# Performance work log

Measured on AMD Instinct MI355X. Metric: run time of the kernel, lower is better.

## Reference

```python
import jax, jax.numpy as jnp
import numpy as np

EMBED_DIM = 768
NUM_HEADS = 12


def setup_inputs() -> dict:
    key = jax.random.key(0)
    k_x, k_w1, k_b1, k_w2, k_b2 = jax.random.split(key, 5)
    B, S, D = 4, 2048, EMBED_DIM
    s1 = 1.0 / np.sqrt(D)
    return {
        "x": jax.random.normal(k_x, (B, S, D), dtype=jnp.float32),
        "W1": jax.random.uniform(k_w1, (D, 3 * D), jnp.float32, -s1, s1),  # proj1 weight (in,out)
        "b1": jax.random.uniform(k_b1, (3 * D,), jnp.float32, -s1, s1),
        "W2": jax.random.uniform(k_w2, (D, D), jnp.float32, -s1, s1),  # proj2 weight (in,out)
        "b2": jax.random.uniform(k_b2, (D,), jnp.float32, -s1, s1),
    }


def reference(x, W1, b1, W2, b2):
    B, S, D = x.shape
    H = NUM_HEADS
    h = D // H
    qkv = x @ W1 + b1                       # [B,S,3D]
    qkv = qkv.reshape(B, S, H, 3 * h).transpose(0, 2, 1, 3)  # [B,H,S,3h]
    # chunk order in the original: K, Q, V
    K = qkv[..., :h]
    Q = qkv[..., h:2 * h]
    V = qkv[..., 2 * h:]
    # NOTE: original code computes Q @ V^T (not Q @ K^T) -- reproduced faithfully
    scores = jnp.einsum("bhqd,bhkd->bhqk", Q, V) / jnp.sqrt(jnp.float32(h))
    att = jax.nn.softmax(scores, axis=-1)
    out = jnp.einsum("bhqk,bhkd->bhqd", att, V)  # [B,H,S,h]
    out = out.transpose(0, 2, 1, 3).reshape(B, S, D)
    return out @ W2 + b2
```

## Files before the change

kernel.cpp:

```cpp
#include <hip/hip_runtime.h>
#include <hip/hip_bf16.h>
#include <math.h>


#define SEQ   2048
#define DIM   768
#define NHEAD 12
#define HDIM  64
#define BATCH 4

#define QSCALE 0.1803368801111244f

typedef __attribute__((ext_vector_type(8))) short s16x8;
typedef __attribute__((ext_vector_type(4))) float f32x4;

#if __has_builtin(__builtin_amdgcn_exp2f)
#define EXP2F(x) __builtin_amdgcn_exp2f(x)
#else
#define EXP2F(x) exp2f(x)
#endif

__device__ __forceinline__ unsigned short f2bf(float f) {
    union { float f; unsigned int u; } v; v.f = f;
    unsigned int r = v.u + 0x7fffu + ((v.u >> 16) & 1u);
    return (unsigned short)(r >> 16);
}

__device__ __forceinline__ void gload_lds16(const void* g, void* l) {
    __builtin_amdgcn_global_load_lds(
        (const __attribute__((address_space(1))) unsigned int*)g,
        (__attribute__((address_space(3))) unsigned int*)l, 16, 0, 0);
}

__global__ __launch_bounds__(256) void cvt_x(const float* __restrict__ x,
                                             unsigned short* __restrict__ xb)
{
    const size_t i4 = ((size_t)blockIdx.x * 256 + threadIdx.x) * 4;
    float4 v = *(const float4*)&x[i4];
    ushort4 o;
    o.x = f2bf(v.x); o.y = f2bf(v.y); o.z = f2bf(v.z); o.w = f2bf(v.w);
    *(ushort4*)&xb[i4] = o;
}

__global__ __launch_bounds__(256) void cvt_wt(const float* __restrict__ W,
                                              unsigned short* __restrict__ out,
                                              int src_ld, int qvmap)
{
    __shared__ float T[32][33];
    const int n0 = blockIdx.x * 32, k0 = blockIdx.y * 32;
    const int c0 = qvmap ? ((n0 >> 7) * 192 + 64 + (n0 & 127)) : n0;
    const int tc = threadIdx.x & 31, tr = threadIdx.x >> 5;
    #pragma unroll
    for (int i = 0; i < 4; ++i)
        T[tr + i * 8][tc] = W[(size_t)(k0 + tr + i * 8) * src_ld + c0 + tc];
    __syncthreads();
    #pragma unroll
    for (int i = 0; i < 4; ++i)
        out[(size_t)(n0 + tr + i * 8) * DIM + k0 + tc] = f2bf(T[tc][tr + i * 8]);
}

__device__ __forceinline__ void gemm128_loop(
    const unsigned short* __restrict__ A, const unsigned short* __restrict__ B,
    unsigned short* As, unsigned short* Bs, int m0, int n0, f32x4 acc[4][4])
{
    const int tid  = threadIdx.x;
    const int wave = tid >> 6;
    const int lane = tid & 63;
    const int quad = lane >> 4;
    const int lcol = lane & 15;
    const int wm = wave >> 1, wn = wave & 1;

    const int sr = lane >> 2;
    const int sp = lane & 3;
    const int sc = sp ^ ((sr >> 1) & 3);

    const int aswz = ((quad ^ ((lcol >> 1) & 3)) << 4);

    for (int k0 = 0; k0 < DIM; k0 += 32) {
        #pragma unroll
        for (int s = 0; s < 2; ++s) {
            const int r0 = wave * 32 + s * 16;
            gload_lds16(&A[(size_t)(m0 + r0 + sr) * DIM + k0 + sc * 8],
                        (void*)&As[r0 * 32]);
            gload_lds16(&B[(size_t)(n0 + r0 + sr) * DIM + k0 + sc * 8],
                        (void*)&Bs[r0 * 32]);
        }
        __syncthreads();

        s16x8 af[4], bf[4];
        #pragma unroll
        for (int mt = 0; mt < 4; ++mt) {
            const int row = wm * 64 + mt * 16 + lcol;
            af[mt] = *(const s16x8*)((const char*)As + row * 64 + aswz);
        }
        #pragma unroll
        for (int nt = 0; nt < 4; ++nt) {
            const int row = wn * 64 + nt * 16 + lcol;
            bf[nt] = *(const s16x8*)((const char*)Bs + row * 64 + aswz);
        }
        #pragma unroll
        for (int mt = 0; mt < 4; ++mt)
            #pragma unroll
            for (int nt = 0; nt < 4; ++nt)
                acc[mt][nt] = __builtin_amdgcn_mfma_f32_16x16x32_bf16(
                    af[mt], bf[nt], acc[mt][nt], 0, 0, 0);
        __syncthreads();
    }
}

__global__ __launch_bounds__(256) void qkv_gemm_bf16(
    const unsigned short* __restrict__ xb, const unsigned short* __restrict__ W1bt,
    const float* __restrict__ b1, unsigned short* __restrict__ Qb,
    unsigned short* __restrict__ Vr, unsigned short* __restrict__ Vt)
{
    __shared__ unsigned short LDSBUF[8192];
    f32x4 acc[4][4] = {};
    const int m0 = blockIdx.y * 128, n0 = blockIdx.x * 128;
    gemm128_loop(xb, W1bt, LDSBUF, LDSBUF + 4096, m0, n0, acc);

    const int tid  = threadIdx.x;
    const int wave = tid >> 6, lane = tid & 63;
    const int quad = lane >> 4, lcol = lane & 15;
    const int wm = wave >> 1, wn = wave & 1;

    const int colblock = n0 + wn * 64;
    const int head = colblock >> 7;
    const int cc0  = colblock & 127;
    const int isQ  = (cc0 == 0);
    const float scale = isQ ? QSCALE : 1.0f;
    unsigned short* dst = isQ ? Qb : Vr;

    float bias[4];
    #pragma unroll
    for (int nt = 0; nt < 4; ++nt)
        bias[nt] = b1[head * 192 + 64 + cc0 + nt * 16 + lcol];

    unsigned short* Wst = LDSBUF + wave * 2048;

    #pragma unroll
    for (int half = 0; half < 2; ++half) {
        #pragma unroll
        for (int mh = 0; mh < 2; ++mh) {
            const int mt = half * 2 + mh;
            #pragma unroll
            for (int nt = 0; nt < 4; ++nt)
                #pragma unroll
                for (int r = 0; r < 4; ++r) {
                    const float v = (acc[mt][nt][r] + bias[nt]) * scale;
                    Wst[(mh * 16 + quad * 4 + r) * 64 + nt * 16 + lcol] = f2bf(v);
                }
        }
        __syncthreads();
        #pragma unroll
        for (int p = 0; p < 4; ++p) {
            const int lr = p * 8 + (lane >> 3);
            const int c8 = (lane & 7) * 8;
            s16x8 v = *(const s16x8*)&Wst[lr * 64 + c8];
            const int m  = m0 + wm * 64 + half * 32 + lr;
            const int bb = m >> 11;
            const int s  = m & 2047;
            const int bhh = bb * NHEAD + head;
            *(s16x8*)&dst[((size_t)bhh * SEQ + s) * HDIM + c8] = v;
        }
        __syncthreads();
    }

    if (!isQ) {
        #pragma unroll
        for (int nt = 0; nt < 4; ++nt) {
            const int d = nt * 16 + lcol;
            #pragma unroll
            for (int mt = 0; mt < 4; ++mt) {
                const int m0r = m0 + wm * 64 + mt * 16 + quad * 4;
                const int bb  = m0r >> 11;
                const int s0  = m0r & 2047;
                const int bhh = bb * NHEAD + head;
                ushort4 o;
                o.x = f2bf(acc[mt][nt][0] + bias[nt]);
                o.y = f2bf(acc[mt][nt][1] + bias[nt]);
                o.z = f2bf(acc[mt][nt][2] + bias[nt]);
                o.w = f2bf(acc[mt][nt][3] + bias[nt]);
                *(ushort4*)&Vt[((size_t)bhh * HDIM + d) * SEQ + s0] = o;
            }
        }
    }
}

__global__ __launch_bounds__(256) void attn_mfma(
    const unsigned short* __restrict__ Qb, const unsigned short* __restrict__ Vr,
    const unsigned short* __restrict__ Vt, unsigned short* __restrict__ Yb)
{
    __shared__ unsigned short VrS[2][64 * 64];
    __shared__ unsigned short VtS[2][64 * 64];
    __shared__ unsigned short Ps[4][32 * 72];

    const int bh = blockIdx.y;
    const int b  = bh / NHEAD;
    const int hh = bh % NHEAD;
    const int q0 = blockIdx.x * 128;

    const int tid  = threadIdx.x;
    const int wave = tid >> 6;
    const int lane = tid & 63;
    const int quad = lane >> 4;
    const int lcol = lane & 15;

    s16x8 qa[2][2];
    #pragma unroll
    for (int mt = 0; mt < 2; ++mt)
        #pragma unroll
        for (int kk = 0; kk < 2; ++kk)
            qa[mt][kk] = *(const s16x8*)&Qb[((size_t)bh * SEQ + q0 + wave * 32 + mt * 16 + lcol) * HDIM
                                            + kk * 32 + quad * 8];

    s16x8 ones;
    #pragma unroll
    for (int i = 0; i < 8; ++i) ones[i] = (short)0x3F80;

    f32x4 oacc[2][4] = {};
    f32x4 lsum[2] = {};

    const int srow = lane >> 3;
    const int schk = (lane & 7) ^ srow;

    for (int k0 = 0; k0 < SEQ; k0 += 128) {
        #pragma unroll
        for (int hf = 0; hf < 2; ++hf)
            #pragma unroll
            for (int s = 0; s < 2; ++s) {
                const int r0 = wave * 16 + s * 8;
                gload_lds16(&Vr[((size_t)bh * SEQ + k0 + hf * 64 + r0 + srow) * HDIM + schk * 8],
                            (void*)&VrS[hf][r0 * 64]);
                gload_lds16(&Vt[((size_t)bh * HDIM + r0 + srow) * SEQ + k0 + hf * 64 + schk * 8],
                            (void*)&VtS[hf][r0 * 64]);
            }
        __syncthreads();

        #pragma unroll
        for (int hf = 0; hf < 2; ++hf) {
            f32x4 sacc[2][4] = {};
            #pragma unroll
            for (int kk = 0; kk < 2; ++kk) {
                s16x8 bf[4];
                #pragma unroll
                for (int nt = 0; nt < 4; ++nt) {
                    const int r = nt * 16 + lcol;
                    const int c = kk * 4 + quad;
                    bf[nt] = *(const s16x8*)((const char*)VrS[hf] + r * 128 + ((c ^ (r & 7)) << 4));
                }
                #pragma unroll
                for (int mt = 0; mt < 2; ++mt)
                    #pragma unroll
                    for (int nt = 0; nt < 4; ++nt)
                        sacc[mt][nt] = __builtin_amdgcn_mfma_f32_16x16x32_bf16(
                            qa[mt][kk], bf[nt], sacc[mt][nt], 0, 0, 0);
            }

            #pragma unroll
            for (int mt = 0; mt < 2; ++mt)
                #pragma unroll
                for (int nt = 0; nt < 4; ++nt)
                    #pragma unroll
                    for (int r = 0; r < 4; ++r) {
                        const float p = EXP2F(sacc[mt][nt][r]);
                        Ps[wave][(mt * 16 + quad * 4 + r) * 72 + nt * 16 + lcol] = f2bf(p);
                    }

            #pragma unroll
            for (int kk = 0; kk < 2; ++kk) {
                s16x8 pa[2];
                #pragma unroll
                for (int mt = 0; mt < 2; ++mt)
                    pa[mt] = *(const s16x8*)&Ps[wave][(mt * 16 + lcol) * 72 + kk * 32 + quad * 8];
                #pragma unroll
                for (int mt = 0; mt < 2; ++mt)
                    lsum[mt] = __builtin_amdgcn_mfma_f32_16x16x32_bf16(
                        pa[mt], ones, lsum[mt], 0, 0, 0);
                #pragma unroll
                for (int dt = 0; dt < 4; ++dt) {
                    const int r = dt * 16 + lcol;
                    const int c = kk * 4 + quad;
                    s16x8 vb = *(const s16x8*)((const char*)VtS[hf] + r * 128 + ((c ^ (r & 7)) << 4));
                    #pragma unroll
                    for (int mt = 0; mt < 2; ++mt)
                        oacc[mt][dt] = __builtin_amdgcn_mfma_f32_16x16x32_bf16(
                            pa[mt], vb, oacc[mt][dt], 0, 0, 0);
                }
            }
        }
        __syncthreads();
    }

    #pragma unroll
    for (int mt = 0; mt < 2; ++mt)
        #pragma unroll
        for (int r = 0; r < 4; ++r) {
            const float invl = 1.0f / lsum[mt][r];
            const int qrow = q0 + wave * 32 + mt * 16 + quad * 4 + r;
            #pragma unroll
            for (int dt = 0; dt < 4; ++dt)
                Yb[((size_t)b * SEQ + qrow) * DIM + hh * HDIM + dt * 16 + lcol] =
                    f2bf(oacc[mt][dt][r] * invl);
        }
}

__global__ __launch_bounds__(256) void proj_gemm_bf16(
    const unsigned short* __restrict__ Yb, const unsigned short* __restrict__ W2bt,
    const float* __restrict__ b2, float* __restrict__ out)
{
    __shared__ unsigned short LDSBUF[8192];
    unsigned short* As = LDSBUF;
    unsigned short* Bs = LDSBUF + 2048;

    const int tid  = threadIdx.x;
    const int wave = tid >> 6;
    const int lane = tid & 63;
    const int quad = lane >> 4;
    const int lcol = lane & 15;
    const int wm = wave >> 1, wn = wave & 1;

    const int m0 = blockIdx.y * 64, n0 = blockIdx.x * 128;

    const int sr = lane >> 2;
    const int sp = lane & 3;
    const int sc = sp ^ ((sr >> 1) & 3);
    const int aswz = ((quad ^ ((lcol >> 1) & 3)) << 4);

    f32x4 acc[2][4] = {};

    for (int k0 = 0; k0 < DIM; k0 += 32) {
        {
            const int r0 = wave * 16;
            gload_lds16(&Yb[(size_t)(m0 + r0 + sr) * DIM + k0 + sc * 8],
                        (void*)&As[r0 * 32]);
        }
        #pragma unroll
        for (int s = 0; s < 2; ++s) {
            const int r0 = wave * 32 + s * 16;
            gload_lds16(&W2bt[(size_t)(n0 + r0 + sr) * DIM + k0 + sc * 8],
                        (void*)&Bs[r0 * 32]);
        }
        __syncthreads();

        s16x8 af[2], bf[4];
        #pragma unroll
        for (int mt = 0; mt < 2; ++mt) {
            const int row = wm * 32 + mt * 16 + lcol;
            af[mt] = *(const s16x8*)((const char*)As + row * 64 + aswz);
        }
        #pragma unroll
        for (int nt = 0; nt < 4; ++nt) {
            const int row = wn * 64 + nt * 16 + lcol;
            bf[nt] = *(const s16x8*)((const char*)Bs + row * 64 + aswz);
        }
        #pragma unroll
        for (int mt = 0; mt < 2; ++mt)
            #pragma unroll
            for (int nt = 0; nt < 4; ++nt)
                acc[mt][nt] = __builtin_amdgcn_mfma_f32_16x16x32_bf16(
                    af[mt], bf[nt], acc[mt][nt], 0, 0, 0);
        __syncthreads();
    }

    float bias[4];
    #pragma unroll
    for (int nt = 0; nt < 4; ++nt)
        bias[nt] = b2[n0 + wn * 64 + nt * 16 + lcol];

    float* W32 = (float*)LDSBUF + wave * 1024;

    #pragma unroll
    for (int mt = 0; mt < 2; ++mt) {
        #pragma unroll
        for (int nt = 0; nt < 4; ++nt)
            #pragma unroll
            for (int r = 0; r < 4; ++r)
                W32[(quad * 4 + r) * 64 + nt * 16 + lcol] = acc[mt][nt][r] + bias[nt];
        __syncthreads();
        #pragma unroll
        for (int p = 0; p < 4; ++p) {
            const int lr = p * 4 + (lane >> 4);
            float4 v = *(const float4*)&W32[lr * 64 + (lane & 15) * 4];
            const int m = m0 + wm * 32 + mt * 16 + lr;
            *(float4*)&out[(size_t)m * DIM + n0 + wn * 64 + (lane & 15) * 4] = v;
        }
        __syncthreads();
    }
}

extern "C" void kernel_launch(void* const* d_in, const int* in_sizes, int n_in,
                              void* d_out, int out_size, void* d_ws, size_t ws_size,
                              hipStream_t stream)
{
    const float* x  = (const float*)d_in[0];
    const float* W1 = (const float*)d_in[1];
    const float* b1 = (const float*)d_in[2];
    const float* W2 = (const float*)d_in[3];
    const float* b2 = (const float*)d_in[4];
    float* out = (float*)d_out;

    const size_t NQV = (size_t)BATCH * NHEAD * SEQ * HDIM;
    unsigned short* Qb   = (unsigned short*)d_ws;
    unsigned short* Vr   = Qb + NQV;
    unsigned short* Vt   = Vr + NQV;
    unsigned short* Yb   = Vt + NQV;
    unsigned short* xb   = Yb + NQV;
    unsigned short* W1bt = xb + NQV;
    unsigned short* W2bt = W1bt + 1536 * DIM;

    cvt_x <<<6144, 256, 0, stream>>>(x, xb);
    cvt_wt<<<dim3(48, 24), 256, 0, stream>>>(W1, W1bt, 2304, 1);
    cvt_wt<<<dim3(24, 24), 256, 0, stream>>>(W2, W2bt, DIM, 0);

    qkv_gemm_bf16<<<dim3(12, 64), 256, 0, stream>>>(xb, W1bt, b1, Qb, Vr, Vt);
    attn_mfma<<<dim3(SEQ / 128, BATCH * NHEAD), 256, 0, stream>>>(Qb, Vr, Vt, Yb);
    proj_gemm_bf16<<<dim3(DIM / 128, 128), 256, 0, stream>>>(Yb, W2bt, b2, out);
}
```

Baseline: 243.5 us.

## Merge conversion kernels, shrink attention KV tile to 64, reorder attention grid

Merges the three fp32-to-bf16 conversion kernels into one launch that dispatches on block index, removing two kernel launches. The attention kernel now stages 64 keys per iteration instead of 128, halving its LDS footprint for higher occupancy at the cost of twice as many barriers. The attention grid is swapped so consecutive blocks cover different heads rather than consecutive query tiles of one head, which changes the L2 reuse pattern for V.

```diff
diff --git a/kernel.cpp b/kernel.cpp
--- a/kernel.cpp
+++ b/kernel.cpp
@@ -32,23 +32,36 @@
         (__attribute__((address_space(3))) unsigned int*)l, 16, 0, 0);
 }
 
-__global__ __launch_bounds__(256) void cvt_x(const float* __restrict__ x,
-                                             unsigned short* __restrict__ xb)
-{
-    const size_t i4 = ((size_t)blockIdx.x * 256 + threadIdx.x) * 4;
-    float4 v = *(const float4*)&x[i4];
-    ushort4 o;
-    o.x = f2bf(v.x); o.y = f2bf(v.y); o.z = f2bf(v.z); o.w = f2bf(v.w);
-    *(ushort4*)&xb[i4] = o;
-}
-
-__global__ __launch_bounds__(256) void cvt_wt(const float* __restrict__ W,
-                                              unsigned short* __restrict__ out,
-                                              int src_ld, int qvmap)
+__global__ __launch_bounds__(256) void cvt_all(
+    const float* __restrict__ x, const float* __restrict__ W1,
+    const float* __restrict__ W2, unsigned short* __restrict__ xb,
+    unsigned short* __restrict__ W1bt, unsigned short* __restrict__ W2bt)
 {
     __shared__ float T[32][33];
-    const int n0 = blockIdx.x * 32, k0 = blockIdx.y * 32;
-    const int c0 = qvmap ? ((n0 >> 7) * 192 + 64 + (n0 & 127)) : n0;
+    const int id = blockIdx.x;
+
+    if (id >= 1728) {
+        const size_t i4 = ((size_t)(id - 1728) * 256 + threadIdx.x) * 4;
+        float4 v = *(const float4*)&x[i4];
+        ushort4 o;
+        o.x = f2bf(v.x); o.y = f2bf(v.y); o.z = f2bf(v.z); o.w = f2bf(v.w);
+        *(ushort4*)&xb[i4] = o;
+        return;
+    }
+
+    const float* W;
+    unsigned short* out;
+    int n0, k0, src_ld, c0;
+    if (id < 1152) {
+        W = W1; out = W1bt; src_ld = 2304;
+        n0 = (id % 48) * 32; k0 = (id / 48) * 32;
+        c0 = (n0 >> 7) * 192 + 64 + (n0 & 127);
+    } else {
+        const int id2 = id - 1152;
+        W = W2; out = W2bt; src_ld = DIM;
+        n0 = (id2 % 24) * 32; k0 = (id2 / 24) * 32;
+        c0 = n0;
+    }
     const int tc = threadIdx.x & 31, tr = threadIdx.x >> 5;
     #pragma unroll
     for (int i = 0; i < 4; ++i)
@@ -190,14 +203,14 @@
     const unsigned short* __restrict__ Qb, const unsigned short* __restrict__ Vr,
     const unsigned short* __restrict__ Vt, unsigned short* __restrict__ Yb)
 {
-    __shared__ unsigned short VrS[2][64 * 64];
-    __shared__ unsigned short VtS[2][64 * 64];
+    __shared__ unsigned short VrS[64 * 64];
+    __shared__ unsigned short VtS[64 * 64];
     __shared__ unsigned short Ps[4][32 * 72];
 
-    const int bh = blockIdx.y;
+    const int bh = blockIdx.x;
     const int b  = bh / NHEAD;
     const int hh = bh % NHEAD;
-    const int q0 = blockIdx.x * 128;
+    const int q0 = blockIdx.y * 128;
 
     const int tid  = threadIdx.x;
     const int wave = tid >> 6;
@@ -223,69 +236,64 @@
     const int srow = lane >> 3;
     const int schk = (lane & 7) ^ srow;
 
-    for (int k0 = 0; k0 < SEQ; k0 += 128) {
-        #pragma unroll
-        for (int hf = 0; hf < 2; ++hf)
-            #pragma unroll
-            for (int s = 0; s < 2; ++s) {
-                const int r0 = wave * 16 + s * 8;
-                gload_lds16(&Vr[((size_t)bh * SEQ + k0 + hf * 64 + r0 + srow) * HDIM + schk * 8],
-                            (void*)&VrS[hf][r0 * 64]);
-                gload_lds16(&Vt[((size_t)bh * HDIM + r0 + srow) * SEQ + k0 + hf * 64 + schk * 8],
-                            (void*)&VtS[hf][r0 * 64]);
+    for (int k0 = 0; k0 < SEQ; k0 += 64) {
+        #pragma unroll
+        for (int s = 0; s < 2; ++s) {
+            const int r0 = wave * 16 + s * 8;
+            gload_lds16(&Vr[((size_t)bh * SEQ + k0 + r0 + srow) * HDIM + schk * 8],
+                        (void*)&VrS[r0 * 64]);
+            gload_lds16(&Vt[((size_t)bh * HDIM + r0 + srow) * SEQ + k0 + schk * 8],
+                        (void*)&VtS[r0 * 64]);
+        }
+        __syncthreads();
+
+        f32x4 sacc[2][4] = {};
+        #pragma unroll
+        for (int kk = 0; kk < 2; ++kk) {
+            s16x8 bf[4];
+            #pragma unroll
+            for (int nt = 0; nt < 4; ++nt) {
+                const int r = nt * 16 + lcol;
+                const int c = kk * 4 + quad;
+                bf[nt] = *(const s16x8*)((const char*)VrS + r * 128 + ((c ^ (r & 7)) << 4));
             }
-        __syncthreads();
-
-        #pragma unroll
-        for (int hf = 0; hf < 2; ++hf) {
-            f32x4 sacc[2][4] = {};
-            #pragma unroll
-            for (int kk = 0; kk < 2; ++kk) {
-                s16x8 bf[4];
-                #pragma unroll
-                for (int nt = 0; nt < 4; ++nt) {
-                    const int r = nt * 16 + lcol;
-                    const int c = kk * 4 + quad;
-                    bf[nt] = *(const s16x8*)((const char*)VrS[hf] + r * 128 + ((c ^ (r & 7)) << 4));
-                }
-                #pragma unroll
-                for (int mt = 0; mt < 2; ++mt)
-                    #pragma unroll
-                    for (int nt = 0; nt < 4; ++nt)
-                        sacc[mt][nt] = __builtin_amdgcn_mfma_f32_16x16x32_bf16(
-                            qa[mt][kk], bf[nt], sacc[mt][nt], 0, 0, 0);
-            }
-
             #pragma unroll
             for (int mt = 0; mt < 2; ++mt)
                 #pragma unroll
                 for (int nt = 0; nt < 4; ++nt)
-                    #pragma unroll
-                    for (int r = 0; r < 4; ++r) {
-                        const float p = EXP2F(sacc[mt][nt][r]);
-                        Ps[wave][(mt * 16 + quad * 4 + r) * 72 + nt * 16 + lcol] = f2bf(p);
-                    }
-
-            #pragma unroll
-            for (int kk = 0; kk < 2; ++kk) {
-                s16x8 pa[2];
+                    sacc[mt][nt] = __builtin_amdgcn_mfma_f32_16x16x32_bf16(
+                        qa[mt][kk], bf[nt], sacc[mt][nt], 0, 0, 0);
+        }
+
+        #pragma unroll
+        for (int mt = 0; mt < 2; ++mt)
+            #pragma unroll
+            for (int nt = 0; nt < 4; ++nt)
+                #pragma unroll
+                for (int r = 0; r < 4; ++r) {
+                    const float p = EXP2F(sacc[mt][nt][r]);
+                    Ps[wave][(mt * 16 + quad * 4 + r) * 72 + nt * 16 + lcol] = f2bf(p);
+                }
+
+        #pragma unroll
+        for (int kk = 0; kk < 2; ++kk) {
+            s16x8 pa[2];
+            #pragma unroll
+            for (int mt = 0; mt < 2; ++mt)
+                pa[mt] = *(const s16x8*)&Ps[wave][(mt * 16 + lcol) * 72 + kk * 32 + quad * 8];
+            #pragma unroll
+            for (int mt = 0; mt < 2; ++mt)
+                lsum[mt] = __builtin_amdgcn_mfma_f32_16x16x32_bf16(
+                    pa[mt], ones, lsum[mt], 0, 0, 0);
+            #pragma unroll
+            for (int dt = 0; dt < 4; ++dt) {
+                const int r = dt * 16 + lcol;
+                const int c = kk * 4 + quad;
+                s16x8 vb = *(const s16x8*)((const char*)VtS + r * 128 + ((c ^ (r & 7)) << 4));
                 #pragma unroll
                 for (int mt = 0; mt < 2; ++mt)
-                    pa[mt] = *(const s16x8*)&Ps[wave][(mt * 16 + lcol) * 72 + kk * 32 + quad * 8];
-                #pragma unroll
-                for (int mt = 0; mt < 2; ++mt)
-                    lsum[mt] = __builtin_amdgcn_mfma_f32_16x16x32_bf16(
-                        pa[mt], ones, lsum[mt], 0, 0, 0);
-                #pragma unroll
-                for (int dt = 0; dt < 4; ++dt) {
-                    const int r = dt * 16 + lcol;
-                    const int c = kk * 4 + quad;
-                    s16x8 vb = *(const s16x8*)((const char*)VtS[hf] + r * 128 + ((c ^ (r & 7)) << 4));
-                    #pragma unroll
-                    for (int mt = 0; mt < 2; ++mt)
-                        oacc[mt][dt] = __builtin_amdgcn_mfma_f32_16x16x32_bf16(
-                            pa[mt], vb, oacc[mt][dt], 0, 0, 0);
-                }
+                    oacc[mt][dt] = __builtin_amdgcn_mfma_f32_16x16x32_bf16(
+                        pa[mt], vb, oacc[mt][dt], 0, 0, 0);
             }
         }
         __syncthreads();
@@ -408,11 +416,9 @@
     unsigned short* W1bt = xb + NQV;
     unsigned short* W2bt = W1bt + 1536 * DIM;
 
-    cvt_x <<<6144, 256, 0, stream>>>(x, xb);
-    cvt_wt<<<dim3(48, 24), 256, 0, stream>>>(W1, W1bt, 2304, 1);
-    cvt_wt<<<dim3(24, 24), 256, 0, stream>>>(W2, W2bt, DIM, 0);
+    cvt_all<<<7872, 256, 0, stream>>>(x, W1, W2, xb, W1bt, W2bt);
 
     qkv_gemm_bf16<<<dim3(12, 64), 256, 0, stream>>>(xb, W1bt, b1, Qb, Vr, Vt);
-    attn_mfma<<<dim3(SEQ / 128, BATCH * NHEAD), 256, 0, stream>>>(Qb, Vr, Vt, Yb);
+    attn_mfma<<<dim3(BATCH * NHEAD, SEQ / 128), 256, 0, stream>>>(Qb, Vr, Vt, Yb);
     proj_gemm_bf16<<<dim3(DIM / 128, 128), 256, 0, stream>>>(Yb, W2bt, b2, out);
 }
```

Measured after the change: 218.2 us. 1.12x faster.
